# Performance work log

Hardware: AMD Instinct MI355X
Metric: run time of the kernel (lower is better)

Reference implementation:

```python
import jax, jax.numpy as jnp
import numpy as np

N, B, NPM = 16384, 256, 64          # nodes, molecules, nodes per molecule
E = 65536                           # edges
FMAX, AMAX = 32, 16                 # FG slots per molecule, atoms per FG
HID, FGE, POSE = 960, 512, 128
NFG, MAXTOK, NFEAT = 205, 160, 5


def setup_inputs() -> dict:
    key = jax.random.key(0)
    ks = jax.random.split(key, 12)
    graph_x = jax.random.normal(ks[0], (N, NFEAT), jnp.float32)
    edge_index = jax.random.randint(ks[1], (2, E), 0, N)
    graph_batch = jnp.arange(N) // NPM
    ptr = jnp.arange(B + 1) * NPM
    fg_type_tensor = jax.random.randint(ks[2], (B, FMAX), 0, NFG)
    idx = jax.random.randint(ks[3], (B, FMAX, AMAX), 0, NPM)
    drop = jax.random.uniform(ks[4], (B, FMAX, AMAX)) < 0.3
    fg_indices_tensor = jnp.where(drop, -1, idx)
    s = lambda k, sh: jax.random.normal(k, sh, jnp.float32) * 0.02
    return dict(
        graph_x=graph_x, edge_index=edge_index, graph_batch=graph_batch, ptr=ptr,
        fg_type_tensor=fg_type_tensor, fg_indices_tensor=fg_indices_tensor,
        W1=s(ks[5], (NFEAT, HID)), b1=jnp.zeros((HID,), jnp.float32),
        W2=s(ks[6], (HID, HID)), b2=jnp.zeros((HID,), jnp.float32),
        fg_embed=s(ks[7], (NFG, FGE)), pos_embed=s(ks[8], (MAXTOK, POSE)),
        projW=s(ks[9], (HID, HID)), projb=jnp.zeros((HID,), jnp.float32),
        fuseW=s(ks[10], (FGE + POSE + HID + HID, HID)), fuseb=jnp.zeros((HID,), jnp.float32),
    )


def gcn_conv(x, W, b, src, dst, n):
    # PyG GCNConv: linear, add self-loops, symmetric deg^-1/2 normalization, sum-aggregate, bias
    h = x @ W
    deg = 1.0 + jax.ops.segment_sum(jnp.ones(src.shape[0], h.dtype), dst, num_segments=n)
    dinv = jax.lax.rsqrt(deg)
    msg = h[src] * (dinv[src] * dinv[dst])[:, None]            # [E, HID]
    out = jax.ops.segment_sum(msg, dst, num_segments=n) + h * (dinv * dinv)[:, None]
    return out + b


def reference(graph_x, edge_index, graph_batch, ptr, fg_type_tensor, fg_indices_tensor,
              W1, b1, W2, b2, fg_embed, pos_embed, projW, projb, fuseW, fuseb):
    src, dst = edge_index[0], edge_index[1]
    n = graph_x.shape[0]
    h = jax.nn.relu(gcn_conv(graph_x, W1, b1, src, dst, n))
    h = gcn_conv(h, W2, b2, src, dst, n)

    Bsz, Fmax = fg_type_tensor.shape
    # global mean pool per molecule
    cnt = jax.ops.segment_sum(jnp.ones(n, h.dtype), graph_batch, num_segments=Bsz)
    global_emb = jax.ops.segment_sum(h, graph_batch, num_segments=Bsz) / cnt[:, None]

    fg_static = fg_embed[fg_type_tensor]                        # [B, F, FGE]
    fg_pos = jnp.broadcast_to(pos_embed[:Fmax][None], (Bsz, Fmax, pos_embed.shape[1]))

    # vectorized FG-specific node pooling (replaces nested python loops)
    mask = fg_indices_tensor >= 0                               # [B, F, A]
    gids = jnp.where(mask, ptr[:-1][:, None, None] + fg_indices_tensor, 0)
    gathered = h[gids] * mask[..., None].astype(h.dtype)        # [B, F, A, HID]
    counts = mask.sum(-1).astype(h.dtype)                       # [B, F]
    pooled = gathered.sum(-2) / jnp.maximum(counts, 1.0)[..., None]
    fg_valid_mask = counts > 0

    fg_node_proj = pooled @ projW + projb
    global_exp = jnp.broadcast_to(global_emb[:, None, :], (Bsz, Fmax, global_emb.shape[1]))
    fused = jnp.concatenate([fg_static, fg_pos, fg_node_proj, global_exp], axis=-1)
    fg_fused = fused @ fuseW + fuseb
    return fg_fused, fg_valid_mask
```

## Files before the change

### kernel.cpp

```cpp
#include <hip/hip_runtime.h>

typedef unsigned short u16;
typedef unsigned int u32;
typedef __attribute__((ext_vector_type(8))) short short8;
typedef __attribute__((ext_vector_type(4))) float f32x4;

#define N_NODES 16384
#define B_MOL   256
#define NPM     64
#define E_EDGES 65536
#define FMAXF   32
#define AMAXA   16
#define HID     960
#define NFG     205
#define BF_ROWS 8192
#define OUT1    7864320
#define NTOT    4516800

__device__ __forceinline__ float bf2f(u16 u){ u32 x=((u32)u)<<16; float f; __builtin_memcpy(&f,&x,4); return f; }
__device__ __forceinline__ u16 f2bf(float f){ u32 x; __builtin_memcpy(&x,&f,4); x += 0x7FFFu + ((x>>16)&1u); return (u16)(x>>16); }

__device__ __forceinline__ void gload_lds16(const u16* g, u16* l){
    __builtin_amdgcn_global_load_lds(
        (const __attribute__((address_space(1))) void*)g,
        (__attribute__((address_space(3))) void*)l, 16, 0, 0);
}
__device__ __forceinline__ size_t swzA(int row, int col){
    return ((size_t)((row>>4)*30 + (col>>5)))*512 + (size_t)(((((col>>3)&3)*16) + (row&15))*8);
}
__device__ __forceinline__ size_t swzE(int row, int col){
    return ((size_t)((row>>4)*30 + (col>>5)))*512 + (size_t)((((col>>3)&3)*16 + (row&15))*8 + (col&7));
}

struct NormSrcs { const void* p[11]; };
__global__ __launch_bounds__(256) void k_normAll(NormSrcs s, u16* __restrict__ region,
                                                 float* __restrict__ b2f, float* __restrict__ projbf,
                                                 float* __restrict__ z4, int* __restrict__ flag,
                                                 int* __restrict__ deg){
    __shared__ int cnt;
    int t = threadIdx.x;
    if (t==0) cnt = 0;
    __syncthreads();
    u16 pv = ((const u16*)s.p[0])[t*2];
    if (((pv>>7)&0xFF) >= 0xC0) atomicAdd(&cnt, 1);
    __syncthreads();
    int fl = (cnt > 16) ? 1 : 0;
    int gid = blockIdx.x*256 + t;
    if (blockIdx.x==0 && t==0) *flag = fl;
    int base = gid*8;
    const f32x4 zf = {0.f,0.f,0.f,0.f};
    if (base < N_NODES){ *(f32x4*)(deg+base) = zf; *(f32x4*)(deg+base+4) = zf; }
    if (base < 4*HID)  { *(f32x4*)(z4+base)  = zf; *(f32x4*)(z4+base+4)  = zf; }
    if (base >= NTOT) return;
    int seg, off;
    if      (base <   81920){seg=0;  off=base;}
    else if (base <   86720){seg=1;  off=base-81920;}
    else if (base <   87680){seg=2;  off=base-86720;}
    else if (base < 1009280){seg=3;  off=base-87680;}
    else if (base < 1010240){seg=4;  off=base-1009280;}
    else if (base < 1115200){seg=5;  off=base-1010240;}
    else if (base < 1135680){seg=6;  off=base-1115200;}
    else if (base < 2057280){seg=7;  off=base-1135680;}
    else if (base < 2058240){seg=8;  off=base-2057280;}
    else if (base < 4515840){seg=9;  off=base-2058240;}
    else                    {seg=10; off=base-4515840;}
    const void* sp = s.p[seg];
    short8 ov;
    float fvs[8];
    if (fl){
        const float* fp = (const float*)sp + off;
        f32x4 v0 = *(const f32x4*)(fp);
        f32x4 v1 = *(const f32x4*)(fp+4);
        #pragma unroll
        for (int j=0;j<4;j++){ fvs[j]=v0[j]; fvs[4+j]=v1[j]; }
        #pragma unroll
        for (int j=0;j<8;j++) ((u16*)&ov)[j] = f2bf(fvs[j]);
    } else {
        ov = *(const short8*)((const u16*)sp + off);
        #pragma unroll
        for (int j=0;j<8;j++) fvs[j] = bf2f(((u16*)&ov)[j]);
    }
    *(short8*)(region + base) = ov;
    if (seg==4){
        *(f32x4*)(b2f+off)   = (f32x4){fvs[0],fvs[1],fvs[2],fvs[3]};
        *(f32x4*)(b2f+off+4) = (f32x4){fvs[4],fvs[5],fvs[6],fvs[7]};
    }
    if (seg==8){
        *(f32x4*)(projbf+off)   = (f32x4){fvs[0],fvs[1],fvs[2],fvs[3]};
        *(f32x4*)(projbf+off+4) = (f32x4){fvs[4],fvs[5],fvs[6],fvs[7]};
    }
}


__device__ __forceinline__ void gemm_sq(int bx, int by, const u16* __restrict__ A, int lda,
                                        const u16* __restrict__ Bt, int ldb,
                                        u16* __restrict__ C, int swz, char* smem)
{
    u16* As = (u16*)smem;
    u16* Bs = (u16*)smem + 64*40;
    const int tid = threadIdx.x;
    const int wave = tid>>6, lane = tid&63;
    const int wm = wave>>1, wn = wave&1;
    const int q = lane>>4, l16 = lane&15;
    const int m0 = bx*64, n0 = by*64;
    const int sm = tid>>2, sk = (tid&3)*8;
    f32x4 acc00={0,0,0,0}, acc01={0,0,0,0}, acc10={0,0,0,0}, acc11={0,0,0,0};
    const u16* Ap = A + (size_t)(m0+sm)*lda + sk;
    const u16* Bp = Bt + (size_t)(n0+sm)*ldb + sk;
    short8 av = *(const short8*)(Ap);
    short8 bv = *(const short8*)(Bp);
    for (int k0=0; k0<HID; k0+=32){
        *(short8*)(As + sm*40 + sk) = av;
        *(short8*)(Bs + sm*40 + sk) = bv;
        __syncthreads();
        if (k0+32 < HID){
            av = *(const short8*)(Ap + k0 + 32);
            bv = *(const short8*)(Bp + k0 + 32);
        }
        short8 a0 = *(const short8*)(As + (wm*32      + l16)*40 + q*8);
        short8 a1 = *(const short8*)(As + (wm*32 + 16 + l16)*40 + q*8);
        short8 b0 = *(const short8*)(Bs + (wn*32      + l16)*40 + q*8);
        short8 b1 = *(const short8*)(Bs + (wn*32 + 16 + l16)*40 + q*8);
        acc00 = __builtin_amdgcn_mfma_f32_16x16x32_bf16(a0,b0,acc00,0,0,0);
        acc01 = __builtin_amdgcn_mfma_f32_16x16x32_bf16(a0,b1,acc01,0,0,0);
        acc10 = __builtin_amdgcn_mfma_f32_16x16x32_bf16(a1,b0,acc10,0,0,0);
        acc11 = __builtin_amdgcn_mfma_f32_16x16x32_bf16(a1,b1,acc11,0,0,0);
        __syncthreads();
    }
    #pragma unroll
    for (int i=0;i<2;i++){
        int rowb = m0 + wm*32 + i*16 + q*4;
        #pragma unroll
        for (int j=0;j<2;j++){
            int col = n0 + wn*32 + j*16 + l16;
            f32x4 av2 = (i==0) ? ((j==0)?acc00:acc01) : ((j==0)?acc10:acc11);
            #pragma unroll
            for (int r=0;r<4;r++){
                int row = rowb + r;
                u16 o = f2bf(av2[r]);
                if (swz) C[swzE(row,col)] = o;
                else     C[(size_t)row*HID + col] = o;
            }
        }
    }
}
__device__ __forceinline__ void gemm64f(int bx, int by, const u16* __restrict__ A, int lda,
                                        const u16* __restrict__ Bt, int ldb,
                                        float* __restrict__ C, int M, int K,
                                        const float* __restrict__ addv, char* smem)
{
    u16* As = (u16*)smem;
    u16* Bs = (u16*)smem + 64*40;
    const int tid = threadIdx.x;
    const int wave = tid>>6, lane = tid&63;
    const int wm = wave>>1, wn = wave&1;
    const int q = lane>>4, l16 = lane&15;
    const int m0 = bx*64, n0 = by*64;
    const int sm = tid>>2, sk = (tid&3)*8;
    f32x4 acc00={0,0,0,0}, acc01={0,0,0,0}, acc10={0,0,0,0}, acc11={0,0,0,0};
    const bool aOk = (m0+sm) < M;
    const u16* Ap = A + (size_t)(m0+sm)*lda + sk;
    const u16* Bp = Bt + (size_t)(n0+sm)*ldb + sk;
    short8 av = {0,0,0,0,0,0,0,0};
    if (aOk) av = *(const short8*)(Ap);
    short8 bv = *(const short8*)(Bp);
    for (int k0=0; k0<K; k0+=32){
        *(short8*)(As + sm*40 + sk) = av;
        *(short8*)(Bs + sm*40 + sk) = bv;
        __syncthreads();
        if (k0+32 < K){
            if (aOk) av = *(const short8*)(Ap + k0 + 32);
            bv = *(const short8*)(Bp + k0 + 32);
        }
        short8 a0 = *(const short8*)(As + (wm*32      + l16)*40 + q*8);
        short8 a1 = *(const short8*)(As + (wm*32 + 16 + l16)*40 + q*8);
        short8 b0 = *(const short8*)(Bs + (wn*32      + l16)*40 + q*8);
        short8 b1 = *(const short8*)(Bs + (wn*32 + 16 + l16)*40 + q*8);
        acc00 = __builtin_amdgcn_mfma_f32_16x16x32_bf16(a0,b0,acc00,0,0,0);
        acc01 = __builtin_amdgcn_mfma_f32_16x16x32_bf16(a0,b1,acc01,0,0,0);
        acc10 = __builtin_amdgcn_mfma_f32_16x16x32_bf16(a1,b0,acc10,0,0,0);
        acc11 = __builtin_amdgcn_mfma_f32_16x16x32_bf16(a1,b1,acc11,0,0,0);
        __syncthreads();
    }
    #pragma unroll
    for (int i=0;i<2;i++){
        int rowb = m0 + wm*32 + i*16 + q*4;
        #pragma unroll
        for (int j=0;j<2;j++){
            int col = n0 + wn*32 + j*16 + l16;
            f32x4 av2 = (i==0) ? ((j==0)?acc00:acc01) : ((j==0)?acc10:acc11);
            float add = addv ? addv[col] : 0.f;
            #pragma unroll
            for (int r=0;r<4;r++){
                int row = rowb + r;
                if (row < M) C[(size_t)row*HID + col] = av2[r] + add;
            }
        }
    }
}
__device__ __forceinline__ void transpose_tile(int bx, int by, const u16* __restrict__ src,
                                               u16* __restrict__ dst, int R, int C, char* smem)
{
    u16 (*tl)[33] = (u16(*)[33])smem;
    int c0 = bx*32, r0 = by*32;
    int tx = threadIdx.x & 31, ty = threadIdx.x >> 5;
    #pragma unroll
    for (int i=0;i<4;i++) tl[ty+i*8][tx] = src[(size_t)(r0+ty+i*8)*C + c0+tx];
    __syncthreads();
    #pragma unroll
    for (int i=0;i<4;i++) dst[(size_t)(c0+ty+i*8)*R + r0+tx] = tl[tx][ty+i*8];
}
__device__ __forceinline__ void vecmat_body(int bx, int by, const float* __restrict__ v,
                                            const u16* __restrict__ M, float* __restrict__ out, char* smem)
{
    float (*part)[64] = (float(*)[64])smem;
    int tid = threadIdx.x;
    int cl = tid & 63;
    int c = bx*64 + cl;
    int kg = tid >> 6;
    int k0 = by*60 + kg*15;
    float s = 0.f;
    #pragma unroll
    for (int i=0;i<15;i++) s += v[k0+i]*bf2f(M[(size_t)(k0+i)*HID + c]);
    part[kg][cl] = s;
    __syncthreads();
    if (kg==0) atomicAdd(&out[c], part[0][cl]+part[1][cl]+part[2][cl]+part[3][cl]);
}
__device__ __forceinline__ void scandinv_body(const int* __restrict__ deg, int* __restrict__ off,
                                              int* __restrict__ cur, float* __restrict__ dinv, char* smem)
{
    int* ps = (int*)smem;
    int t = threadIdx.x;
    const int chunk = N_NODES/256;
    int base0 = t*chunk;
    int s = 0;
    for (int i=0;i<chunk;i++) s += deg[base0+i];
    ps[t] = s; __syncthreads();
    for (int ofs=1; ofs<256; ofs<<=1){
        int v = ps[t];
        int add = (t>=ofs) ? ps[t-ofs] : 0;
        __syncthreads();
        ps[t] = v + add;
        __syncthreads();
    }
    int run = (t==0) ? 0 : ps[t-1];
    for (int i=0;i<chunk;i++){
        int d = deg[base0+i];
        off[base0+i]=run; cur[base0+i]=run; run += d;
        dinv[base0+i] = rsqrtf(1.0f + (float)d);
    }
    if (t==255) off[N_NODES] = run;
}

__global__ __launch_bounds__(256) void k_L1(const u16* __restrict__ fuseWn, u16* __restrict__ fuseWT,
                                            const int* __restrict__ dst, int* __restrict__ deg){
    __shared__ __attribute__((aligned(16))) char smem[2112];
    int b = blockIdx.x;
    if (b < 2400){
        transpose_tile(b%30, b/30, fuseWn, fuseWT, 2560, HID, smem);
    } else {
        int e = (b-2400)*256 + threadIdx.x;
        if (e < E_EDGES) atomicAdd(&deg[dst[e]], 1);
    }
}
__global__ __launch_bounds__(256) void k_L2(const u16* fuseWT, const u16* projWn, const u16* W2n,
                                            u16* Ub, u16* WglobT,
                                            const int* deg, int* off, int* cur, float* dinv){
    __shared__ __attribute__((aligned(16))) char smem[10240];
    int b = blockIdx.x;
    if (b < 450){
        int z = b/225, r = b%225;
        if (z==0) gemm_sq(r%15, r/15, fuseWT+640, 2560, projWn, HID, Ub, 0, smem);
        else      gemm_sq(r%15, r/15, fuseWT+1600, 2560, W2n, HID, WglobT, 0, smem);
    } else {
        scandinv_body(deg, off, cur, dinv, smem);
    }
}
__global__ __launch_bounds__(256) void k_L3(const u16* Ub, const u16* W2n, u16* WbigS,
                                            const u16* fgeN, const u16* posN, const u16* fuseWT,
                                            float* fgA, float* pWbM,
                                            const int* src, const int* dst, const float* dinv,
                                            int* cur, int* csr_s, float* csr_w){
    __shared__ __attribute__((aligned(16))) char smem[10240];
    int b = blockIdx.x;
    if (b < 225){
        gemm_sq(b%15, b/15, Ub, HID, W2n, HID, WbigS, 1, smem);
    } else if (b < 300){
        int bb = b-225;
        if (bb < 60) gemm64f(bb%4, bb/4, fgeN, 512, fuseWT, 2560, fgA, NFG, 512, nullptr, smem);
        else         gemm64f(0, bb-60, posN, 128, fuseWT+512, 2560, pWbM, FMAXF, 128, nullptr, smem);
    } else {
        int e = (b-300)*256 + threadIdx.x;
        if (e < E_EDGES){
            int s = src[e], d = dst[e];
            int p = atomicAdd(&cur[d], 1);
            csr_s[p] = s;
            csr_w[p] = dinv[s]*dinv[d];
        }
    }
}
__global__ __launch_bounds__(256) void k_L4(const u16* __restrict__ gxn, const float* __restrict__ dinv,
                                            const int* __restrict__ off, const int* __restrict__ csr_s,
                                            const float* __restrict__ csr_w,
                                            const u16* __restrict__ W1, const u16* __restrict__ b1,
                                            u16* __restrict__ h1b,
                                            const float* b2f, const float* projbf, const u16* fuseWn,
                                            const u16* projWn, float* tvb, float* cC, float* gvec){
    __shared__ __attribute__((aligned(16))) char smem[1024];
    int b = blockIdx.x;
    if (b < 8192){
        float* a2 = (float*)smem;
        int t = threadIdx.x;
        int h = t>>7, tl = t&127;
        int n = b*2 + h;
        if (tl < 5){
            int k = tl;
            float di = dinv[n], sw = di*di;
            float a = sw * bf2f(gxn[n*5+k]);
            int j0 = off[n], j1 = off[n+1];
            for (int j=j0;j<j1;j++) a += csr_w[j]*bf2f(gxn[csr_s[j]*5+k]);
            a2[h*8+k] = a;
        }
        __syncthreads();
        if (tl < 120){
            int c8 = tl*8;
            float a[5];
            #pragma unroll
            for (int k=0;k<5;k++) a[k] = a2[h*8+k];
            float r[8];
            short8 bb = *(const short8*)(b1 + c8);
            #pragma unroll
            for (int j=0;j<8;j++) r[j] = bf2f(((u16*)&bb)[j]);
            #pragma unroll
            for (int k=0;k<5;k++){
                short8 wv = *(const short8*)(W1 + k*HID + c8);
                #pragma unroll
                for (int j=0;j<8;j++) r[j] += a[k]*bf2f(((u16*)&wv)[j]);
            }
            short8 o;
            #pragma unroll
            for (int j=0;j<8;j++) ((u16*)&o)[j] = f2bf(fmaxf(r[j],0.f));
            *(short8*)(h1b + (size_t)n*HID + c8) = o;
        }
    } else {
        int bb = b - 8192;
        int z = bb/240, r = bb%240;
        if (z==0)      vecmat_body(r%15, r/15, b2f,    projWn,            tvb,  smem);
        else if (z==1) vecmat_body(r%15, r/15, projbf, fuseWn + 640*HID,  cC,   smem);
        else           vecmat_body(r%15, r/15, b2f,    fuseWn + 1600*HID, gvec, smem);
    }
}
__global__ __launch_bounds__(256) void k_L5(const u16* __restrict__ h1b, const float* __restrict__ dinv,
                                            const int* __restrict__ off, const int* __restrict__ csr_s,
                                            const float* __restrict__ csr_w, u16* __restrict__ P1b,
                                            const float* tvb, const u16* fuseWn, float* vb,
                                            const float* cC, const float* gvec, const u16* fusebn, float* c0){
    __shared__ __attribute__((aligned(16))) char smem[1024];
    int b = blockIdx.x;
    if (b < 4096){
        int wv = threadIdx.x>>6, lane = threadIdx.x&63;
        int n = b*4 + wv;
        int c = lane*16;
        bool act = lane < 60;
        float di = dinv[n], sw = di*di;
        float acc[16];
        if (act){
            short8 h0 = *(const short8*)(h1b + (size_t)n*HID + c);
            short8 h1v = *(const short8*)(h1b + (size_t)n*HID + c + 8);
            #pragma unroll
            for (int j=0;j<8;j++){ acc[j] = sw*bf2f(((u16*)&h0)[j]); acc[8+j] = sw*bf2f(((u16*)&h1v)[j]); }
        } else {
            #pragma unroll
            for (int j=0;j<16;j++) acc[j] = 0.f;
        }
        int j0 = off[n], j1 = off[n+1];
        for (int j=j0;j<j1;j++){
            int s = csr_s[j]; float w = csr_w[j];
            if (act){
                short8 v0 = *(const short8*)(h1b + (size_t)s*HID + c);
                short8 v1 = *(const short8*)(h1b + (size_t)s*HID + c + 8);
                #pragma unroll
                for (int j2=0;j2<8;j2++){ acc[j2] += w*bf2f(((u16*)&v0)[j2]); acc[8+j2] += w*bf2f(((u16*)&v1)[j2]); }
            }
        }
        if (act){
            short8 o0, o1;
            #pragma unroll
            for (int j=0;j<8;j++){ ((u16*)&o0)[j] = f2bf(acc[j]); ((u16*)&o1)[j] = f2bf(acc[8+j]); }
            *(short8*)(P1b + (size_t)n*HID + c) = o0;
            *(short8*)(P1b + (size_t)n*HID + c + 8) = o1;
        }
    } else if (b < 4336){
        int bb = b - 4096;
        vecmat_body(bb%15, bb/15, tvb, fuseWn + 640*HID, vb, smem);
    } else {
        int c = (b-4336)*256 + threadIdx.x;
        if (c < HID) c0[c] = cC[c] + gvec[c] + bf2f(fusebn[c]);
    }
}
__global__ __launch_bounds__(256) void k_L6(const u16* __restrict__ P1b, const int* __restrict__ fgi,
                                            const int* __restrict__ ptr, u16* __restrict__ prb,
                                            float* __restrict__ evec, u16* __restrict__ maskb,
                                            float* __restrict__ maskf, const int* __restrict__ flag,
                                            u16* __restrict__ gmb){
    int b = blockIdx.x;
    if (b < 2048){
        int wv = threadIdx.x>>6, lane = threadIdx.x&63;
        int bf = b*4 + wv;
        int mb = bf >> 5;
        int base = ptr[mb];
        int c = lane*16;
        bool act = lane < 60;
        float acc[16];
        #pragma unroll
        for (int j=0;j<16;j++) acc[j] = 0.f;
        int cnt = 0;
        #pragma unroll
        for (int a=0;a<AMAXA;a++){
            int idx = fgi[bf*AMAXA + a];
            if (idx >= 0){
                cnt++;
                if (act){
                    short8 v0 = *(const short8*)(P1b + (size_t)(base+idx)*HID + c);
                    short8 v1 = *(const short8*)(P1b + (size_t)(base+idx)*HID + c + 8);
                    #pragma unroll
                    for (int j=0;j<8;j++){ acc[j] += bf2f(((u16*)&v0)[j]); acc[8+j] += bf2f(((u16*)&v1)[j]); }
                }
            }
        }
        float inv = (cnt>0) ? 1.0f/(float)cnt : 0.0f;
        if (act){
            short8 o0, o1;
            #pragma unroll
            for (int j=0;j<8;j++){ ((u16*)&o0)[j] = f2bf(acc[j]*inv); ((u16*)&o1)[j] = f2bf(acc[8+j]*inv); }
            *(short8*)(prb + swzA(bf, c)) = o0;
            *(short8*)(prb + swzA(bf, c+8)) = o1;
        }
        if (lane == 0){
            float e = (cnt>0) ? 1.0f : 0.0f;
            evec[bf] = e;
            if (*flag) maskf[bf] = e;
            else       maskb[bf] = f2bf(e);
        }
    } else {
        int id = (b-2048)*256 + threadIdx.x;
        int mb = id / 120; int c8 = (id - mb*120)*8;
        float s[8] = {0,0,0,0,0,0,0,0};
        for (int i=0;i<NPM;i++){
            short8 v = *(const short8*)(P1b + (size_t)(mb*NPM+i)*HID + c8);
            #pragma unroll
            for (int j=0;j<8;j++) s[j] += bf2f(((u16*)&v)[j]);
        }
        const float inv = 1.0f/(float)NPM;
        short8 o;
        #pragma unroll
        for (int j=0;j<8;j++) ((u16*)&o)[j] = f2bf(s[j]*inv);
        *(short8*)(gmb + (size_t)mb*HID + c8) = o;
    }
}
__global__ __launch_bounds__(256) void k_L7(const u16* gmb, const u16* WglobT, float* Gc, const float* c0){
    __shared__ __attribute__((aligned(16))) char smem[10240];
    int b = blockIdx.x;
    gemm64f(b%4, b/4, gmb, HID, WglobT, HID, Gc, B_MOL, HID, c0, smem);
}

__global__ __launch_bounds__(256) void k_gemmF(
    const u16* __restrict__ A, const u16* __restrict__ Bt,
    float* __restrict__ Cf, u16* __restrict__ Cb,
    const int* __restrict__ fg_type, const float* __restrict__ evec,
    const float* __restrict__ fgA, const float* __restrict__ pWbM,
    const float* __restrict__ vb, const float* __restrict__ Gc,
    const int* __restrict__ flag)
{
    __shared__ __attribute__((aligned(16))) u16 S[3][14*512];
    const int tid = threadIdx.x;
    const int wave = tid>>6, lane = tid&63;
    const int wm = wave>>1, wn = wave&1;
    const int q = lane>>4, l16 = lane&15;
    const int m0 = blockIdx.x*128, n0 = blockIdx.y*96;
    const int R0 = blockIdx.x*8, N0 = blockIdx.y*6;

    f32x4 acc[4][3];
    #pragma unroll
    for (int i=0;i<4;i++)
        #pragma unroll
        for (int j=0;j<3;j++) acc[i][j] = (f32x4){0,0,0,0};

    const int isf = *flag;
    int tyv[16]; float evv[16];
    #pragma unroll
    for (int i=0;i<4;i++)
        #pragma unroll
        for (int r=0;r<4;r++){
            int row = m0 + wm*64 + i*16 + q*4 + r;
            tyv[i*4+r] = fg_type[row];
            evv[i*4+r] = evec[row];
        }
    asm volatile("s_waitcnt vmcnt(0)" ::: "memory");

    const u16* gA0 = A  + ((size_t)(R0 + wave*2    )*30)*512 + lane*8;
    const u16* gA1 = A  + ((size_t)(R0 + wave*2 + 1)*30)*512 + lane*8;
    const u16* gB0 = Bt + ((size_t)(N0 + wave      )*30)*512 + lane*8;
    const u16* gB1 = Bt + ((size_t)(N0 + 4 + wave  )*30)*512 + lane*8;

    u16* sA = &S[0][0];
    u16* sB = &S[1][0];
    u16* sC = &S[2][0];

    {
        gload_lds16(gA0, sA + (wave*2  )*512);
        gload_lds16(gA1, sA + (wave*2+1)*512);
        gload_lds16(gB0, sA + (8+wave)*512);
        if (wave < 2) gload_lds16(gB1, sA + (12+wave)*512);
        const int kn = 512;
        gload_lds16(gA0 + kn, sB + (wave*2  )*512);
        gload_lds16(gA1 + kn, sB + (wave*2+1)*512);
        gload_lds16(gB0 + kn, sB + (8+wave)*512);
        if (wave < 2) gload_lds16(gB1 + kn, sB + (12+wave)*512);
    }
    if (wave < 2) asm volatile("s_waitcnt vmcnt(4)" ::: "memory");
    else          asm volatile("s_waitcnt vmcnt(3)" ::: "memory");
    __builtin_amdgcn_s_barrier();

    for (int kc=0; kc<30; kc++){
        if (kc+2 < 30){
            const int kn = (kc+2)*512;
            gload_lds16(gA0 + kn, sC + (wave*2  )*512);
            gload_lds16(gA1 + kn, sC + (wave*2+1)*512);
            gload_lds16(gB0 + kn, sC + (8+wave)*512);
            if (wave < 2) gload_lds16(gB1 + kn, sC + (12+wave)*512);
        }
        short8 af[4], bfr[3];
        #pragma unroll
        for (int i=0;i<4;i++) af[i] = *(const short8*)(sA + (wm*4+i)*512 + lane*8);
        #pragma unroll
        for (int j=0;j<3;j++) bfr[j] = *(const short8*)(sA + (8+wn*3+j)*512 + lane*8);
        __builtin_amdgcn_s_setprio(1);
        #pragma unroll
        for (int i=0;i<4;i++)
            #pragma unroll
            for (int j=0;j<3;j++)
                acc[i][j] = __builtin_amdgcn_mfma_f32_16x16x32_bf16(af[i], bfr[j], acc[i][j], 0,0,0);
        __builtin_amdgcn_s_setprio(0);
        if (kc < 29){
            if (kc < 28){
                if (wave < 2) asm volatile("s_waitcnt vmcnt(4)" ::: "memory");
                else          asm volatile("s_waitcnt vmcnt(3)" ::: "memory");
            } else {
                asm volatile("s_waitcnt vmcnt(0)" ::: "memory");
            }
            __builtin_amdgcn_s_barrier();
        }
        u16* t = sA; sA = sB; sB = sC; sC = t;
    }

    #pragma unroll
    for (int j=0;j<3;j++){
        int col = n0 + wn*48 + j*16 + l16;
        float vbc = vb[col];
        #pragma unroll
        for (int i=0;i<4;i++){
            int rowb = m0 + wm*64 + i*16 + q*4;
            float gcv = Gc[(size_t)(rowb>>5)*HID + col];
            #pragma unroll
            for (int r=0;r<4;r++){
                int row = rowb + r;
                int ff = row&31;
                int ty = tyv[i*4+r];
                float e = evv[i*4+r];
                float v = acc[i][j][r]
                        + fgA[(size_t)ty*HID+col] + pWbM[ff*HID+col]
                        + e*vbc + gcv;
                if (isf) Cf[(size_t)row*HID + col] = v;
                else     Cb[(size_t)row*HID + col] = f2bf(v);
            }
        }
    }
}

extern "C" void kernel_launch(void* const* d_in, const int* in_sizes, int n_in,
                              void* d_out, int out_size, void* d_ws, size_t ws_size,
                              hipStream_t stream) {
    const int* edge_idx  = (const int*)d_in[1];
    const int* ptr       = (const int*)d_in[3];
    const int* fg_type   = (const int*)d_in[4];
    const int* fg_idx    = (const int*)d_in[5];

    char* w = (char*)d_ws;
    auto nxt = [&](size_t b)->char*{ char* p = w; w += (b + 255) & ~(size_t)255; return p; };
    u16* big0   = (u16*)nxt((size_t)N_NODES*HID*2);
    u16* fuseWT = big0;
    u16* Ub     = big0 + (size_t)HID*2560;
    u16* h1b    = big0;
    u16* prb    = big0;
    u16* P1b    = (u16*)nxt((size_t)N_NODES*HID*2);
    u16*  WbigS  = (u16*) nxt((size_t)HID*HID*2);
    u16*  WglobT = (u16*) nxt((size_t)HID*HID*2);
    float* fgA   = (float*)nxt((size_t)NFG*HID*4);
    float* pWbM  = (float*)nxt((size_t)FMAXF*HID*4);
    float* b2f   = (float*)nxt(HID*4);
    float* projbf= (float*)nxt(HID*4);
    float* tvb   = (float*)nxt(HID*4);
    float* cC    = (float*)nxt(HID*4);
    float* gvec  = (float*)nxt(HID*4);
    float* vb    = (float*)nxt(HID*4);
    float* c0    = (float*)nxt(HID*4);
    int*   deg   = (int*)  nxt(N_NODES*4);
    float* dinv  = (float*)nxt(N_NODES*4);
    int*   off   = (int*)  nxt((N_NODES+1)*4);
    int*   cur   = (int*)  nxt(N_NODES*4);
    int*   csr_s = (int*)  nxt(E_EDGES*4);
    float* csr_w = (float*)nxt(E_EDGES*4);
    float* evec  = (float*)nxt(BF_ROWS*4);
    u16*   gmb   = (u16*)  nxt((size_t)B_MOL*HID*2);
    float* Gc    = (float*)nxt((size_t)B_MOL*HID*4);
    int*   flag  = (int*)  nxt(256);
    u16*   region= (u16*)  nxt((size_t)NTOT*2);
    u16* gxn    = region;
    u16* W1n    = region +   81920;
    u16* b1n    = region +   86720;
    u16* W2n    = region +   87680;
    u16* fgeN   = region + 1010240;
    u16* posN   = region + 1115200;
    u16* projWn = region + 1135680;
    u16* fuseWn = region + 2058240;
    u16* fusebn = region + 4515840;

    NormSrcs ns;
    ns.p[0]=d_in[0]; ns.p[1]=d_in[6]; ns.p[2]=d_in[7]; ns.p[3]=d_in[8]; ns.p[4]=d_in[9];
    ns.p[5]=d_in[10]; ns.p[6]=d_in[11]; ns.p[7]=d_in[12]; ns.p[8]=d_in[13]; ns.p[9]=d_in[14]; ns.p[10]=d_in[15];
    k_normAll<<<(NTOT/8+255)/256,256,0,stream>>>(ns, region, b2f, projbf, tvb, flag, deg);
    k_L1<<<2656,256,0,stream>>>(fuseWn, fuseWT, edge_idx + E_EDGES, deg);
    k_L2<<<451,256,0,stream>>>(fuseWT, projWn, W2n, Ub, WglobT, deg, off, cur, dinv);
    k_L3<<<556,256,0,stream>>>(Ub, W2n, WbigS, fgeN, posN, fuseWT, fgA, pWbM,
                               edge_idx, edge_idx + E_EDGES, dinv, cur, csr_s, csr_w);
    k_L4<<<8912,256,0,stream>>>(gxn, dinv, off, csr_s, csr_w, W1n, b1n, h1b,
                                b2f, projbf, fuseWn, projWn, tvb, cC, gvec);
    k_L5<<<4340,256,0,stream>>>(h1b, dinv, off, csr_s, csr_w, P1b,
                                tvb, fuseWn, vb, cC, gvec, fusebn, c0);
    k_L6<<<2168,256,0,stream>>>(P1b, fg_idx, ptr, prb, evec,
                                (u16*)d_out + OUT1, (float*)d_out + OUT1, flag, gmb);
    k_L7<<<60,256,0,stream>>>(gmb, WglobT, Gc, c0);
    k_gemmF<<<dim3(64,10),256,0,stream>>>(prb, WbigS, (float*)d_out, (u16*)d_out,
                                          fg_type, evec, fgA, pWbM, vb, Gc, flag);
    (void)in_sizes; (void)n_in; (void)out_size; (void)ws_size;
}
```

Baseline: 291.5 us.

## Split-K global GEMM with atomics, split mean-pool across lanes, defer epilogue loads

Measured after the change: 273.1 us. 6.3% less time.

```diff
diff --git a/kernel.cpp b/kernel.cpp
--- a/kernel.cpp
+++ b/kernel.cpp
@@ -147,7 +147,7 @@
 __device__ __forceinline__ void gemm64f(int bx, int by, const u16* __restrict__ A, int lda,
                                         const u16* __restrict__ Bt, int ldb,
                                         float* __restrict__ C, int M, int K,
-                                        const float* __restrict__ addv, char* smem)
+                                        const float* __restrict__ addv, int atom, char* smem)
 {
     u16* As = (u16*)smem;
     u16* Bs = (u16*)smem + 64*40;
@@ -193,7 +193,11 @@
             #pragma unroll
             for (int r=0;r<4;r++){
                 int row = rowb + r;
-                if (row < M) C[(size_t)row*HID + col] = av2[r] + add;
+                if (row < M){
+                    float v = av2[r] + add;
+                    if (atom) atomicAdd(&C[(size_t)row*HID + col], v);
+                    else      C[(size_t)row*HID + col] = v;
+                }
             }
         }
     }
@@ -287,8 +291,8 @@
         gemm_sq(b%15, b/15, Ub, HID, W2n, HID, WbigS, 1, smem);
     } else if (b < 300){
         int bb = b-225;
-        if (bb < 60) gemm64f(bb%4, bb/4, fgeN, 512, fuseWT, 2560, fgA, NFG, 512, nullptr, smem);
-        else         gemm64f(0, bb-60, posN, 128, fuseWT+512, 2560, pWbM, FMAXF, 128, nullptr, smem);
+        if (bb < 60) gemm64f(bb%4, bb/4, fgeN, 512, fuseWT, 2560, fgA, NFG, 512, nullptr, 0, smem);
+        else         gemm64f(0, bb-60, posN, 128, fuseWT+512, 2560, pWbM, FMAXF, 128, nullptr, 0, smem);
     } else {
         int e = (b-300)*256 + threadIdx.x;
         if (e < E_EDGES){
@@ -354,7 +358,8 @@
                                             const int* __restrict__ off, const int* __restrict__ csr_s,
                                             const float* __restrict__ csr_w, u16* __restrict__ P1b,
                                             const float* tvb, const u16* fuseWn, float* vb,
-                                            const float* cC, const float* gvec, const u16* fusebn, float* c0){
+                                            const float* cC, const float* gvec, const u16* fusebn, float* c0,
+                                            float* __restrict__ Gc){
     __shared__ __attribute__((aligned(16))) char smem[1024];
     int b = blockIdx.x;
     if (b < 4096){
@@ -393,9 +398,12 @@
     } else if (b < 4336){
         int bb = b - 4096;
         vecmat_body(bb%15, bb/15, tvb, fuseWn + 640*HID, vb, smem);
-    } else {
+    } else if (b < 4340){
         int c = (b-4336)*256 + threadIdx.x;
         if (c < HID) c0[c] = cC[c] + gvec[c] + bf2f(fusebn[c]);
+    } else {
+        int id = (b-4340)*256 + threadIdx.x;
+        *(f32x4*)(Gc + (size_t)id*4) = (f32x4){0.f,0.f,0.f,0.f};
     }
 }
 __global__ __launch_bounds__(256) void k_L6(const u16* __restrict__ P1b, const int* __restrict__ fgi,
@@ -443,25 +451,34 @@
             else       maskb[bf] = f2bf(e);
         }
     } else {
-        int id = (b-2048)*256 + threadIdx.x;
-        int mb = id / 120; int c8 = (id - mb*120)*8;
+        int bb = b - 2048;
+        int idt = bb*256 + threadIdx.x;
+        int item = idt >> 1, half = idt & 1;
+        int mb = item / 120; int c8 = (item - mb*120)*8;
+        const u16* Pp = P1b + (size_t)(mb*NPM + half*32)*HID + c8;
         float s[8] = {0,0,0,0,0,0,0,0};
-        for (int i=0;i<NPM;i++){
-            short8 v = *(const short8*)(P1b + (size_t)(mb*NPM+i)*HID + c8);
+        for (int i=0;i<32;i++){
+            short8 v = *(const short8*)(Pp + (size_t)i*HID);
             #pragma unroll
             for (int j=0;j<8;j++) s[j] += bf2f(((u16*)&v)[j]);
         }
-        const float inv = 1.0f/(float)NPM;
-        short8 o;
-        #pragma unroll
-        for (int j=0;j<8;j++) ((u16*)&o)[j] = f2bf(s[j]*inv);
-        *(short8*)(gmb + (size_t)mb*HID + c8) = o;
+        #pragma unroll
+        for (int j=0;j<8;j++) s[j] += __shfl_xor(s[j], 1, 64);
+        if (half == 0){
+            const float inv = 1.0f/(float)NPM;
+            short8 o;
+            #pragma unroll
+            for (int j=0;j<8;j++) ((u16*)&o)[j] = f2bf(s[j]*inv);
+            *(short8*)(gmb + (size_t)mb*HID + c8) = o;
+        }
     }
 }
 __global__ __launch_bounds__(256) void k_L7(const u16* gmb, const u16* WglobT, float* Gc, const float* c0){
     __shared__ __attribute__((aligned(16))) char smem[10240];
     int b = blockIdx.x;
-    gemm64f(b%4, b/4, gmb, HID, WglobT, HID, Gc, B_MOL, HID, c0, smem);
+    int z = b/60, r = b%60;
+    gemm64f(r%4, r/4, gmb + z*480, HID, WglobT + z*480, HID, Gc, B_MOL, 480,
+            z ? nullptr : c0, 1, smem);
 }
 
 __global__ __launch_bounds__(256) void k_gemmF(
@@ -486,18 +503,6 @@
         #pragma unroll
         for (int j=0;j<3;j++) acc[i][j] = (f32x4){0,0,0,0};
 
-    const int isf = *flag;
-    int tyv[16]; float evv[16];
-    #pragma unroll
-    for (int i=0;i<4;i++)
-        #pragma unroll
-        for (int r=0;r<4;r++){
-            int row = m0 + wm*64 + i*16 + q*4 + r;
-            tyv[i*4+r] = fg_type[row];
-            evv[i*4+r] = evec[row];
-        }
-    asm volatile("s_waitcnt vmcnt(0)" ::: "memory");
-
     const u16* gA0 = A  + ((size_t)(R0 + wave*2    )*30)*512 + lane*8;
     const u16* gA1 = A  + ((size_t)(R0 + wave*2 + 1)*30)*512 + lane*8;
     const u16* gB0 = Bt + ((size_t)(N0 + wave      )*30)*512 + lane*8;
@@ -554,23 +559,22 @@
         u16* t = sA; sA = sB; sB = sC; sC = t;
     }
 
+    const int isf = *flag;
     #pragma unroll
-    for (int j=0;j<3;j++){
-        int col = n0 + wn*48 + j*16 + l16;
-        float vbc = vb[col];
-        #pragma unroll
-        for (int i=0;i<4;i++){
-            int rowb = m0 + wm*64 + i*16 + q*4;
-            float gcv = Gc[(size_t)(rowb>>5)*HID + col];
-            #pragma unroll
-            for (int r=0;r<4;r++){
-                int row = rowb + r;
-                int ff = row&31;
-                int ty = tyv[i*4+r];
-                float e = evv[i*4+r];
+    for (int i=0;i<4;i++){
+        int rowb = m0 + wm*64 + i*16 + q*4;
+        #pragma unroll
+        for (int r=0;r<4;r++){
+            int row = rowb + r;
+            int bb = row>>5, ff = row&31;
+            int ty = fg_type[row];
+            float e = evec[row];
+            #pragma unroll
+            for (int j=0;j<3;j++){
+                int col = n0 + wn*48 + j*16 + l16;
                 float v = acc[i][j][r]
                         + fgA[(size_t)ty*HID+col] + pWbM[ff*HID+col]
-                        + e*vbc + gcv;
+                        + e*vb[col] + Gc[(size_t)bb*HID+col];
                 if (isf) Cf[(size_t)row*HID + col] = v;
                 else     Cb[(size_t)row*HID + col] = f2bf(v);
             }
@@ -636,11 +640,11 @@
                                edge_idx, edge_idx + E_EDGES, dinv, cur, csr_s, csr_w);
     k_L4<<<8912,256,0,stream>>>(gxn, dinv, off, csr_s, csr_w, W1n, b1n, h1b,
                                 b2f, projbf, fuseWn, projWn, tvb, cC, gvec);
-    k_L5<<<4340,256,0,stream>>>(h1b, dinv, off, csr_s, csr_w, P1b,
-                                tvb, fuseWn, vb, cC, gvec, fusebn, c0);
-    k_L6<<<2168,256,0,stream>>>(P1b, fg_idx, ptr, prb, evec,
+    k_L5<<<4580,256,0,stream>>>(h1b, dinv, off, csr_s, csr_w, P1b,
+                                tvb, fuseWn, vb, cC, gvec, fusebn, c0, Gc);
+    k_L6<<<2288,256,0,stream>>>(P1b, fg_idx, ptr, prb, evec,
                                 (u16*)d_out + OUT1, (float*)d_out + OUT1, flag, gmb);
-    k_L7<<<60,256,0,stream>>>(gmb, WglobT, Gc, c0);
+    k_L7<<<120,256,0,stream>>>(gmb, WglobT, Gc, c0);
     k_gemmF<<<dim3(64,10),256,0,stream>>>(prb, WbigS, (float*)d_out, (u16*)d_out,
                                           fg_type, evec, fgA, pWbM, vb, Gc, flag);
     (void)in_sizes; (void)n_in; (void)out_size; (void)ws_size;
```
